# Performance work log

Hardware: AMD Instinct MI355X
Metric: run time of the kernel (lower is better)

## Reference

```python
import jax, jax.numpy as jnp
import numpy as np

B, S, D, DO, L, E = 8, 2048, 256, 256, 8, 32768


def setup_inputs() -> dict:
    key = jax.random.key(0)
    k1, k2, k3, k4, k5, k6 = jax.random.split(key, 6)
    node_repr = jax.random.normal(k1, (B, S, D), dtype=jnp.float32)
    edge_src = jax.random.randint(k2, (B, E), 0, S, dtype=jnp.int32)
    edge_tgt = jax.random.randint(k3, (B, E), 0, S, dtype=jnp.int32)
    edge_label = jax.random.randint(k4, (B, E), 0, L, dtype=jnp.int32)
    # per-label Linear params (torch default: kaiming-ish uniform; values here are random stand-ins)
    bound = 1.0 / np.sqrt(D)
    W = jax.random.uniform(k5, (L, D, DO), dtype=jnp.float32, minval=-bound, maxval=bound)
    b = jax.random.uniform(k6, (L, DO), dtype=jnp.float32, minval=-bound, maxval=bound)
    return {"node_repr": node_repr, "edge_src": edge_src, "edge_tgt": edge_tgt,
            "edge_label": edge_label, "W": W, "b": b}


def reference(node_repr, edge_src, edge_tgt, edge_label, W, b):
    # Transform every node by every label's linear once: y[b,l,s,:] = x[b,s,:] @ W[l] + b[l]
    y = jnp.einsum('bsd,ldo->blso', node_repr, W) + b[None, :, None, :]  # [B,L,S,DO]
    bidx = jnp.arange(node_repr.shape[0])[:, None]                       # [B,1]
    msgs = y[bidx, edge_label, edge_src]                                 # [B,E,DO] gather
    out = jnp.zeros(node_repr.shape[:2] + (W.shape[-1],), dtype=node_repr.dtype)
    out = out.at[bidx, edge_tgt].add(msgs)                               # scatter-add into targets
    return jax.nn.relu(out)
```

## Files before the change

### kernel.cpp

```cpp
#include <hip/hip_runtime.h>
#include <stdint.h>

constexpr int NB = 8;
constexpr int NS = 2048;
constexpr int ND = 256;
constexpr int NDO = 256;
constexpr int NL = 8;
constexpr int NE = 32768;

typedef __attribute__((ext_vector_type(8))) short bf16x8;
typedef __attribute__((ext_vector_type(4))) float f32x4;
typedef unsigned int u32;

__device__ __forceinline__ float bf2f(uint32_t u) {
    return __uint_as_float(u << 16);
}
__device__ __forceinline__ uint16_t f2bf(float f) {
    uint32_t x = __float_as_uint(f);
    uint32_t r = (x + 0x7fffu + ((x >> 16) & 1u)) >> 16;
    return (uint16_t)r;
}

__device__ __forceinline__ void gl_lds16(const void* gptr, void* lptr) {
    __builtin_amdgcn_global_load_lds(
        (const __attribute__((address_space(1))) u32*)gptr,
        (__attribute__((address_space(3))) u32*)lptr, 16, 0, 0);
}

__global__ void convert_x_kernel(const float* __restrict__ x, ushort* __restrict__ xb) {
    int i = blockIdx.x * blockDim.x + threadIdx.x;
    const float4* xv = (const float4*)x;
    float4 v = xv[i];
    ushort4 o;
    o.x = f2bf(v.x); o.y = f2bf(v.y); o.z = f2bf(v.z); o.w = f2bf(v.w);
    ((ushort4*)xb)[i] = o;
}

__global__ void convert_wt_kernel(const float* __restrict__ W, ushort* __restrict__ wt) {
    int i = blockIdx.x * blockDim.x + threadIdx.x;
    int d = i & (ND - 1);
    int o = (i >> 8) & (NDO - 1);
    int l = i >> 16;
    wt[i] = f2bf(W[(size_t)(l * ND + d) * NDO + o]);
}

__global__ void hist_kernel(const int* __restrict__ tgt, int* __restrict__ counts) {
    int i = blockIdx.x * blockDim.x + threadIdx.x;
    int b = i >> 15;
    atomicAdd(&counts[b * NS + tgt[i]], 1);
}

__global__ void scan_kernel(const int* __restrict__ counts,
                            int* __restrict__ offsets, int* __restrict__ cursor) {
    int b = blockIdx.x;
    int t = threadIdx.x;
    __shared__ int part[256];
    int base = b * NS + t * 8;
    int s = 0;
    for (int i = 0; i < 8; i++) s += counts[base + i];
    part[t] = s;
    __syncthreads();
    if (t == 0) {
        int run = 0;
        for (int i = 0; i < 256; i++) { int v = part[i]; part[i] = run; run += v; }
    }
    __syncthreads();
    int run = part[t];
    for (int i = 0; i < 8; i++) {
        offsets[base + i] = run;
        cursor[base + i] = run;
        run += counts[base + i];
    }
}

__global__ void place_kernel(const int* __restrict__ tgt,
                             const int* __restrict__ esrc, const int* __restrict__ elab,
                             int* __restrict__ cursor, int* __restrict__ sorted) {
    int i = blockIdx.x * blockDim.x + threadIdx.x;
    int b = i >> 15;
    int tg = tgt[i];
    int lab = elab[i];
    int src = esrc[i];
    int p = atomicAdd(&cursor[b * NS + tg], 1);
    sorted[b * NE + p] = (b * NL + lab) * NS + src;
}

__global__ __launch_bounds__(256) void gemm_kernel(
    const ushort* __restrict__ xb, const ushort* __restrict__ wt,
    const float* __restrict__ bias, ushort* __restrict__ y) {
    int n0 = blockIdx.x * 128;
    int m0 = blockIdx.y * 128;
    int bl = blockIdx.z;
    int b = bl >> 3;
    int l = bl & 7;

    __shared__ ushort As[128 * 32];
    __shared__ ushort Bs[128 * 32];

    int tid = threadIdx.x;
    int lane = tid & 63;
    int wave = __builtin_amdgcn_readfirstlane(tid >> 6);
    int wm = wave & 1, wn = wave >> 1;
    int ln = lane & 15, quad = lane >> 4;

    f32x4 acc[4][4] = {};

    const ushort* Ag = xb + (size_t)(b * NS + m0) * ND;
    const ushort* Bg = wt + (size_t)(l * NDO + n0) * ND;

    int r0 = tid >> 2, c0 = (tid & 3) << 3;
    int r1 = (256 + tid) >> 2, c1 = c0;

    for (int k0 = 0; k0 < ND; k0 += 32) {
        ushort* lA0 = &As[(wave * 64) * 8];
        ushort* lA1 = &As[(256 + wave * 64) * 8];
        ushort* lB0 = &Bs[(wave * 64) * 8];
        ushort* lB1 = &Bs[(256 + wave * 64) * 8];
        gl_lds16(Ag + (size_t)r0 * ND + k0 + c0, lA0);
        gl_lds16(Ag + (size_t)r1 * ND + k0 + c1, lA1);
        gl_lds16(Bg + (size_t)r0 * ND + k0 + c0, lB0);
        gl_lds16(Bg + (size_t)r1 * ND + k0 + c1, lB1);
        __syncthreads();

        bf16x8 af[4], bfr[4];
        for (int i = 0; i < 4; i++)
            af[i] = *(const bf16x8*)&As[(wm * 64 + i * 16 + ln) * 32 + quad * 8];
        for (int j = 0; j < 4; j++)
            bfr[j] = *(const bf16x8*)&Bs[(wn * 64 + j * 16 + ln) * 32 + quad * 8];
        for (int i = 0; i < 4; i++)
            for (int j = 0; j < 4; j++)
                acc[i][j] = __builtin_amdgcn_mfma_f32_16x16x32_bf16(af[i], bfr[j], acc[i][j], 0, 0, 0);
        __syncthreads();
    }

    ushort* yb = y + (size_t)(b * NL + l) * NS * NDO;
    for (int j = 0; j < 4; j++) {
        int col = n0 + wn * 64 + j * 16 + ln;
        float bv = bias[l * NDO + col];
        for (int i = 0; i < 4; i++) {
            int rbase = m0 + wm * 64 + i * 16 + quad * 4;
            for (int r = 0; r < 4; r++) {
                yb[(size_t)(rbase + r) * NDO + col] = f2bf(acc[i][j][r] + bv);
            }
        }
    }
}

__device__ __forceinline__ void accum4(float4& a, uint2 v) {
    a.x += bf2f(v.x & 0xffffu);
    a.y += bf2f(v.x >> 16);
    a.z += bf2f(v.y & 0xffffu);
    a.w += bf2f(v.y >> 16);
}

__global__ __launch_bounds__(256) void gather_kernel(
    const ushort* __restrict__ y,
    const int* __restrict__ counts, const int* __restrict__ offsets,
    const int* __restrict__ sorted, float* __restrict__ out) {
    int g = blockIdx.x * 4 + (threadIdx.x >> 6);
    int lane = threadIdx.x & 63;
    int b = g >> 11;
    int t = g & (NS - 1);

    int n = counts[b * NS + t];
    int off = offsets[b * NS + t];
    const int* ridx = sorted + (size_t)b * NE + off;

    float4 a0 = {0.f, 0.f, 0.f, 0.f};
    float4 a1 = {0.f, 0.f, 0.f, 0.f};
    float4 a2 = {0.f, 0.f, 0.f, 0.f};
    float4 a3 = {0.f, 0.f, 0.f, 0.f};

    for (int base = 0; base < n; base += 64) {
        int m = n - base;
        if (m > 64) m = 64;
        int my = (lane < m) ? ridx[base + lane] : 0;
        int k = 0;
        for (; k + 4 <= m; k += 4) {
            int i0 = __shfl(my, k);
            int i1 = __shfl(my, k + 1);
            int i2 = __shfl(my, k + 2);
            int i3 = __shfl(my, k + 3);
            uint2 v0 = ((const uint2*)(y + (size_t)i0 * NDO))[lane];
            uint2 v1 = ((const uint2*)(y + (size_t)i1 * NDO))[lane];
            uint2 v2 = ((const uint2*)(y + (size_t)i2 * NDO))[lane];
            uint2 v3 = ((const uint2*)(y + (size_t)i3 * NDO))[lane];
            accum4(a0, v0);
            accum4(a1, v1);
            accum4(a2, v2);
            accum4(a3, v3);
        }
        for (; k < m; k++) {
            int i0 = __shfl(my, k);
            uint2 v0 = ((const uint2*)(y + (size_t)i0 * NDO))[lane];
            accum4(a0, v0);
        }
    }

    float4 r;
    r.x = fmaxf(a0.x + a1.x + a2.x + a3.x, 0.f);
    r.y = fmaxf(a0.y + a1.y + a2.y + a3.y, 0.f);
    r.z = fmaxf(a0.z + a1.z + a2.z + a3.z, 0.f);
    r.w = fmaxf(a0.w + a1.w + a2.w + a3.w, 0.f);
    ((float4*)(out + (size_t)(b * NS + t) * NDO))[lane] = r;
}

extern "C" void kernel_launch(void* const* d_in, const int* in_sizes, int n_in,
                              void* d_out, int out_size, void* d_ws, size_t ws_size,
                              hipStream_t stream) {
    const float* x    = (const float*)d_in[0];
    const int*   esrc = (const int*)d_in[1];
    const int*   etgt = (const int*)d_in[2];
    const int*   elab = (const int*)d_in[3];
    const float* W    = (const float*)d_in[4];
    const float* bias = (const float*)d_in[5];
    float* out = (float*)d_out;

    char* ws = (char*)d_ws;
    ushort* xb     = (ushort*)(ws);
    ushort* wt     = (ushort*)(ws + 8388608);
    ushort* y      = (ushort*)(ws + 9437184);
    int*    counts = (int*)(ws + 76546048);
    int*    offs   = (int*)(ws + 76611584);
    int*    cursor = (int*)(ws + 76677120);
    int*    sorted = (int*)(ws + 76742656);

    hipMemsetAsync(counts, 0, NB * NS * sizeof(int), stream);

    convert_x_kernel<<<4096, 256, 0, stream>>>(x, xb);
    convert_wt_kernel<<<2048, 256, 0, stream>>>(W, wt);
    hist_kernel<<<1024, 256, 0, stream>>>(etgt, counts);
    scan_kernel<<<NB, 256, 0, stream>>>(counts, offs, cursor);
    place_kernel<<<1024, 256, 0, stream>>>(etgt, esrc, elab, cursor, sorted);
    gemm_kernel<<<dim3(2, 16, 64), 256, 0, stream>>>(xb, wt, bias, y);
    gather_kernel<<<4096, 256, 0, stream>>>(y, counts, offs, sorted, out);
}
```

Baseline: 168.4 us.

## Aggregate node features per (target,label) before one concatenated-K GEMM with bias counts

Reorders the computation so raw bf16 node features are summed per (target, label) bucket first, giving H[b,t,l,:]. A single GEMM over K = L*D plus per-label edge counts then applies W and the bias, with ReLU fused into the epilogue. This removes the full B*L*S*DO intermediate y and the gather over it, and folds the conversion kernels and memset into one prep kernel. In exchange the GEMM has K of about 2080 instead of 256, and the aggregated sums and counts are rounded to bf16, which adds precision risk.

```diff
diff --git a/kernel.cpp b/kernel.cpp
--- a/kernel.cpp
+++ b/kernel.cpp
@@ -7,6 +7,8 @@
 constexpr int NDO = 256;
 constexpr int NL = 8;
 constexpr int NE = 32768;
+constexpr int NG = NS * NL;
+constexpr int KH = NL * ND + 32;
 
 typedef __attribute__((ext_vector_type(8))) short bf16x8;
 typedef __attribute__((ext_vector_type(4))) float f32x4;
@@ -15,10 +17,9 @@
 __device__ __forceinline__ float bf2f(uint32_t u) {
     return __uint_as_float(u << 16);
 }
-__device__ __forceinline__ uint16_t f2bf(float f) {
+__device__ __forceinline__ uint32_t f2bf(float f) {
     uint32_t x = __float_as_uint(f);
-    uint32_t r = (x + 0x7fffu + ((x >> 16) & 1u)) >> 16;
-    return (uint16_t)r;
+    return (x + 0x7fffu + ((x >> 16) & 1u)) >> 16;
 }
 
 __device__ __forceinline__ void gl_lds16(const void* gptr, void* lptr) {
@@ -27,37 +28,50 @@
         (__attribute__((address_space(3))) u32*)lptr, 16, 0, 0);
 }
 
-__global__ void convert_x_kernel(const float* __restrict__ x, ushort* __restrict__ xb) {
-    int i = blockIdx.x * blockDim.x + threadIdx.x;
-    const float4* xv = (const float4*)x;
-    float4 v = xv[i];
-    ushort4 o;
-    o.x = f2bf(v.x); o.y = f2bf(v.y); o.z = f2bf(v.z); o.w = f2bf(v.w);
-    ((ushort4*)xb)[i] = o;
-}
-
-__global__ void convert_wt_kernel(const float* __restrict__ W, ushort* __restrict__ wt) {
-    int i = blockIdx.x * blockDim.x + threadIdx.x;
-    int d = i & (ND - 1);
-    int o = (i >> 8) & (NDO - 1);
-    int l = i >> 16;
-    wt[i] = f2bf(W[(size_t)(l * ND + d) * NDO + o]);
-}
-
-__global__ void hist_kernel(const int* __restrict__ tgt, int* __restrict__ counts) {
+__global__ void prep_kernel(const float* __restrict__ x, const float* __restrict__ W,
+                            const float* __restrict__ bias,
+                            ushort* __restrict__ xb, ushort* __restrict__ wt2,
+                            int* __restrict__ counts) {
+    int blk = blockIdx.x;
+    int tid = threadIdx.x;
+    if (blk < 4096) {
+        int i = blk * 256 + tid;
+        float4 v = ((const float4*)x)[i];
+        ushort4 o;
+        o.x = (ushort)f2bf(v.x); o.y = (ushort)f2bf(v.y);
+        o.z = (ushort)f2bf(v.z); o.w = (ushort)f2bf(v.w);
+        ((ushort4*)xb)[i] = o;
+    } else if (blk < 4352) {
+        int o = blk - 4096;
+        for (int k = tid; k < KH; k += 256) {
+            float v = 0.f;
+            if (k < NL * ND) v = W[(size_t)k * NDO + o];
+            else if (k < NL * ND + NL) v = bias[(k - NL * ND) * NDO + o];
+            wt2[(size_t)o * KH + k] = (ushort)f2bf(v);
+        }
+    } else {
+        int i = (blk - 4352) * 256 + tid;
+        ((int4*)counts)[i] = make_int4(0, 0, 0, 0);
+    }
+}
+
+__global__ void hist_kernel(const int* __restrict__ tgt, const int* __restrict__ lab,
+                            int* __restrict__ counts) {
     int i = blockIdx.x * blockDim.x + threadIdx.x;
     int b = i >> 15;
-    atomicAdd(&counts[b * NS + tgt[i]], 1);
+    int g = b * NG + tgt[i] * NL + lab[i];
+    atomicAdd(&counts[g], 1);
 }
 
 __global__ void scan_kernel(const int* __restrict__ counts,
-                            int* __restrict__ offsets, int* __restrict__ cursor) {
+                            int* __restrict__ offsets, int* __restrict__ cursor,
+                            ushort* __restrict__ H) {
     int b = blockIdx.x;
     int t = threadIdx.x;
     __shared__ int part[256];
-    int base = b * NS + t * 8;
+    int base = b * NG + t * 64;
     int s = 0;
-    for (int i = 0; i < 8; i++) s += counts[base + i];
+    for (int i = 0; i < 64; i++) s += counts[base + i];
     part[t] = s;
     __syncthreads();
     if (t == 0) {
@@ -66,36 +80,90 @@
     }
     __syncthreads();
     int run = part[t];
-    for (int i = 0; i < 8; i++) {
+    for (int i = 0; i < 64; i++) {
         offsets[base + i] = run;
         cursor[base + i] = run;
         run += counts[base + i];
     }
-}
-
-__global__ void place_kernel(const int* __restrict__ tgt,
-                             const int* __restrict__ esrc, const int* __restrict__ elab,
+    for (int tt = 0; tt < 8; tt++) {
+        int trow = t * 8 + tt;
+        ushort vals[32] __attribute__((aligned(16)));
+        for (int l = 0; l < NL; l++)
+            vals[l] = (ushort)f2bf((float)counts[b * NG + trow * NL + l]);
+        for (int l = NL; l < 32; l++) vals[l] = 0;
+        ushort* dst = H + ((size_t)(b * NS + trow)) * KH + NL * ND;
+        for (int q = 0; q < 4; q++) ((uint4*)dst)[q] = ((const uint4*)vals)[q];
+    }
+}
+
+__global__ void place_kernel(const int* __restrict__ tgt, const int* __restrict__ lab,
+                             const int* __restrict__ esrc,
                              int* __restrict__ cursor, int* __restrict__ sorted) {
     int i = blockIdx.x * blockDim.x + threadIdx.x;
     int b = i >> 15;
-    int tg = tgt[i];
-    int lab = elab[i];
-    int src = esrc[i];
-    int p = atomicAdd(&cursor[b * NS + tg], 1);
-    sorted[b * NE + p] = (b * NL + lab) * NS + src;
+    int g = b * NG + tgt[i] * NL + lab[i];
+    int p = atomicAdd(&cursor[g], 1);
+    sorted[b * NE + p] = esrc[i];
+}
+
+__device__ __forceinline__ void accum4(float4& a, uint2 v) {
+    a.x += bf2f(v.x & 0xffffu);
+    a.y += bf2f(v.x >> 16);
+    a.z += bf2f(v.y & 0xffffu);
+    a.w += bf2f(v.y >> 16);
+}
+
+__global__ __launch_bounds__(256) void aggregate_kernel(
+    const ushort* __restrict__ xb,
+    const int* __restrict__ counts, const int* __restrict__ offsets,
+    const int* __restrict__ sorted, ushort* __restrict__ H) {
+    int g = blockIdx.x * 4 + (threadIdx.x >> 6);
+    int lane = threadIdx.x & 63;
+    int b = g >> 14;
+    int r = g & (NG - 1);
+    int t = r >> 3, l = r & (NL - 1);
+
+    int n = counts[g];
+    int off = offsets[g];
+    const int* srcs = sorted + (size_t)b * NE + off;
+    const ushort* xbb = xb + (size_t)b * NS * ND;
+
+    float4 a0 = {0.f, 0.f, 0.f, 0.f};
+    float4 a1 = {0.f, 0.f, 0.f, 0.f};
+    for (int base = 0; base < n; base += 64) {
+        int m = n - base;
+        if (m > 64) m = 64;
+        int my = (lane < m) ? srcs[base + lane] : 0;
+        int k = 0;
+        for (; k + 2 <= m; k += 2) {
+            int s0 = __shfl(my, k);
+            int s1 = __shfl(my, k + 1);
+            uint2 v0 = ((const uint2*)(xbb + (size_t)s0 * ND))[lane];
+            uint2 v1 = ((const uint2*)(xbb + (size_t)s1 * ND))[lane];
+            accum4(a0, v0);
+            accum4(a1, v1);
+        }
+        if (k < m) {
+            int s0 = __shfl(my, k);
+            uint2 v0 = ((const uint2*)(xbb + (size_t)s0 * ND))[lane];
+            accum4(a0, v0);
+        }
+    }
+    a0.x += a1.x; a0.y += a1.y; a0.z += a1.z; a0.w += a1.w;
+    uint2 o;
+    o.x = f2bf(a0.x) | (f2bf(a0.y) << 16);
+    o.y = f2bf(a0.z) | (f2bf(a0.w) << 16);
+    ((uint2*)(H + ((size_t)(b * NS + t)) * KH + l * ND))[lane] = o;
 }
 
 __global__ __launch_bounds__(256) void gemm_kernel(
-    const ushort* __restrict__ xb, const ushort* __restrict__ wt,
-    const float* __restrict__ bias, ushort* __restrict__ y) {
-    int n0 = blockIdx.x * 128;
+    const ushort* __restrict__ H, const ushort* __restrict__ wt2,
+    float* __restrict__ out) {
+    int nb0 = blockIdx.x * 64;
     int m0 = blockIdx.y * 128;
-    int bl = blockIdx.z;
-    int b = bl >> 3;
-    int l = bl & 7;
 
     __shared__ ushort As[128 * 32];
-    __shared__ ushort Bs[128 * 32];
+    __shared__ ushort Bs[64 * 32];
 
     int tid = threadIdx.x;
     int lane = tid & 63;
@@ -103,106 +171,40 @@
     int wm = wave & 1, wn = wave >> 1;
     int ln = lane & 15, quad = lane >> 4;
 
-    f32x4 acc[4][4] = {};
-
-    const ushort* Ag = xb + (size_t)(b * NS + m0) * ND;
-    const ushort* Bg = wt + (size_t)(l * NDO + n0) * ND;
-
-    int r0 = tid >> 2, c0 = (tid & 3) << 3;
-    int r1 = (256 + tid) >> 2, c1 = c0;
-
-    for (int k0 = 0; k0 < ND; k0 += 32) {
-        ushort* lA0 = &As[(wave * 64) * 8];
-        ushort* lA1 = &As[(256 + wave * 64) * 8];
-        ushort* lB0 = &Bs[(wave * 64) * 8];
-        ushort* lB1 = &Bs[(256 + wave * 64) * 8];
-        gl_lds16(Ag + (size_t)r0 * ND + k0 + c0, lA0);
-        gl_lds16(Ag + (size_t)r1 * ND + k0 + c1, lA1);
-        gl_lds16(Bg + (size_t)r0 * ND + k0 + c0, lB0);
-        gl_lds16(Bg + (size_t)r1 * ND + k0 + c1, lB1);
+    f32x4 acc[4][2] = {};
+
+    const ushort* Ag = H + (size_t)m0 * KH;
+    const ushort* Bg = wt2 + (size_t)nb0 * KH;
+
+    int ra0 = tid >> 2, ca = (tid & 3) << 3;
+    int ra1 = ra0 + 64;
+
+    for (int k0 = 0; k0 < KH; k0 += 32) {
+        gl_lds16(Ag + (size_t)ra0 * KH + k0 + ca, &As[(wave * 64) * 8]);
+        gl_lds16(Ag + (size_t)ra1 * KH + k0 + ca, &As[(256 + wave * 64) * 8]);
+        gl_lds16(Bg + (size_t)ra0 * KH + k0 + ca, &Bs[(wave * 64) * 8]);
         __syncthreads();
 
-        bf16x8 af[4], bfr[4];
+        bf16x8 af[4], bfr[2];
         for (int i = 0; i < 4; i++)
             af[i] = *(const bf16x8*)&As[(wm * 64 + i * 16 + ln) * 32 + quad * 8];
-        for (int j = 0; j < 4; j++)
-            bfr[j] = *(const bf16x8*)&Bs[(wn * 64 + j * 16 + ln) * 32 + quad * 8];
+        for (int j = 0; j < 2; j++)
+            bfr[j] = *(const bf16x8*)&Bs[(wn * 32 + j * 16 + ln) * 32 + quad * 8];
         for (int i = 0; i < 4; i++)
-            for (int j = 0; j < 4; j++)
+            for (int j = 0; j < 2; j++)
                 acc[i][j] = __builtin_amdgcn_mfma_f32_16x16x32_bf16(af[i], bfr[j], acc[i][j], 0, 0, 0);
         __syncthreads();
     }
 
-    ushort* yb = y + (size_t)(b * NL + l) * NS * NDO;
-    for (int j = 0; j < 4; j++) {
-        int col = n0 + wn * 64 + j * 16 + ln;
-        float bv = bias[l * NDO + col];
+    for (int j = 0; j < 2; j++) {
+        int col = nb0 + wn * 32 + j * 16 + ln;
         for (int i = 0; i < 4; i++) {
             int rbase = m0 + wm * 64 + i * 16 + quad * 4;
-            for (int r = 0; r < 4; r++) {
-                yb[(size_t)(rbase + r) * NDO + col] = f2bf(acc[i][j][r] + bv);
+            for (int rr = 0; rr < 4; rr++) {
+                out[(size_t)(rbase + rr) * NDO + col] = fmaxf(acc[i][j][rr], 0.f);
             }
         }
     }
-}
-
-__device__ __forceinline__ void accum4(float4& a, uint2 v) {
-    a.x += bf2f(v.x & 0xffffu);
-    a.y += bf2f(v.x >> 16);
-    a.z += bf2f(v.y & 0xffffu);
-    a.w += bf2f(v.y >> 16);
-}
-
-__global__ __launch_bounds__(256) void gather_kernel(
-    const ushort* __restrict__ y,
-    const int* __restrict__ counts, const int* __restrict__ offsets,
-    const int* __restrict__ sorted, float* __restrict__ out) {
-    int g = blockIdx.x * 4 + (threadIdx.x >> 6);
-    int lane = threadIdx.x & 63;
-    int b = g >> 11;
-    int t = g & (NS - 1);
-
-    int n = counts[b * NS + t];
-    int off = offsets[b * NS + t];
-    const int* ridx = sorted + (size_t)b * NE + off;
-
-    float4 a0 = {0.f, 0.f, 0.f, 0.f};
-    float4 a1 = {0.f, 0.f, 0.f, 0.f};
-    float4 a2 = {0.f, 0.f, 0.f, 0.f};
-    float4 a3 = {0.f, 0.f, 0.f, 0.f};
-
-    for (int base = 0; base < n; base += 64) {
-        int m = n - base;
-        if (m > 64) m = 64;
-        int my = (lane < m) ? ridx[base + lane] : 0;
-        int k = 0;
-        for (; k + 4 <= m; k += 4) {
-            int i0 = __shfl(my, k);
-            int i1 = __shfl(my, k + 1);
-            int i2 = __shfl(my, k + 2);
-            int i3 = __shfl(my, k + 3);
-            uint2 v0 = ((const uint2*)(y + (size_t)i0 * NDO))[lane];
-            uint2 v1 = ((const uint2*)(y + (size_t)i1 * NDO))[lane];
-            uint2 v2 = ((const uint2*)(y + (size_t)i2 * NDO))[lane];
-            uint2 v3 = ((const uint2*)(y + (size_t)i3 * NDO))[lane];
-            accum4(a0, v0);
-            accum4(a1, v1);
-            accum4(a2, v2);
-            accum4(a3, v3);
-        }
-        for (; k < m; k++) {
-            int i0 = __shfl(my, k);
-            uint2 v0 = ((const uint2*)(y + (size_t)i0 * NDO))[lane];
-            accum4(a0, v0);
-        }
-    }
-
-    float4 r;
-    r.x = fmaxf(a0.x + a1.x + a2.x + a3.x, 0.f);
-    r.y = fmaxf(a0.y + a1.y + a2.y + a3.y, 0.f);
-    r.z = fmaxf(a0.z + a1.z + a2.z + a3.z, 0.f);
-    r.w = fmaxf(a0.w + a1.w + a2.w + a3.w, 0.f);
-    ((float4*)(out + (size_t)(b * NS + t) * NDO))[lane] = r;
 }
 
 extern "C" void kernel_launch(void* const* d_in, const int* in_sizes, int n_in,
@@ -218,20 +220,17 @@
 
     char* ws = (char*)d_ws;
     ushort* xb     = (ushort*)(ws);
-    ushort* wt     = (ushort*)(ws + 8388608);
-    ushort* y      = (ushort*)(ws + 9437184);
-    int*    counts = (int*)(ws + 76546048);
-    int*    offs   = (int*)(ws + 76611584);
-    int*    cursor = (int*)(ws + 76677120);
-    int*    sorted = (int*)(ws + 76742656);
-
-    hipMemsetAsync(counts, 0, NB * NS * sizeof(int), stream);
-
-    convert_x_kernel<<<4096, 256, 0, stream>>>(x, xb);
-    convert_wt_kernel<<<2048, 256, 0, stream>>>(W, wt);
-    hist_kernel<<<1024, 256, 0, stream>>>(etgt, counts);
-    scan_kernel<<<NB, 256, 0, stream>>>(counts, offs, cursor);
-    place_kernel<<<1024, 256, 0, stream>>>(etgt, esrc, elab, cursor, sorted);
-    gemm_kernel<<<dim3(2, 16, 64), 256, 0, stream>>>(xb, wt, bias, y);
-    gather_kernel<<<4096, 256, 0, stream>>>(y, counts, offs, sorted, out);
-}
+    ushort* wt2    = (ushort*)(ws + 8388608);
+    ushort* H      = (ushort*)(ws + 10485760);
+    int*    counts = (int*)(ws + 78643200);
+    int*    offs   = (int*)(ws + 79167488);
+    int*    cursor = (int*)(ws + 79691776);
+    int*    sorted = (int*)(ws + 80216064);
+
+    prep_kernel<<<4480, 256, 0, stream>>>(x, W, bias, xb, wt2, counts);
+    hist_kernel<<<1024, 256, 0, stream>>>(etgt, elab, counts);
+    scan_kernel<<<NB, 256, 0, stream>>>(counts, offs, cursor, H);
+    place_kernel<<<1024, 256, 0, stream>>>(etgt, elab, esrc, cursor, sorted);
+    aggregate_kernel<<<32768, 256, 0, stream>>>(xb, counts, offs, sorted, H);
+    gemm_kernel<<<dim3(4, 128), 256, 0, stream>>>(H, wt2, out);
+}
```

Result: slower. 243.9 us (+44.8%).
